# Performance work log

Measured on AMD Instinct MI355X. Metric: run time of the kernel, lower is better.

Reference implementation:

```python
import jax, jax.numpy as jnp
import numpy as np

INPUT_DIM = 1024
NUM_TARGETS = 128
BATCH = 32768


def setup_inputs() -> dict:
    key = jax.random.key(0)
    kx, kw, kb = jax.random.split(key, 3)
    x = jax.random.normal(kx, (BATCH, INPUT_DIM), dtype=jnp.float32)
    # Fused view of num_targets independent nn.Linear(input_dim, 1) layers:
    # column t of W / entry t of b are the weights/bias of layer t.
    bound = 1.0 / np.sqrt(INPUT_DIM)  # torch Linear default init range
    W = jax.random.uniform(kw, (INPUT_DIM, NUM_TARGETS), minval=-bound, maxval=bound, dtype=jnp.float32)
    b = jax.random.uniform(kb, (NUM_TARGETS,), minval=-bound, maxval=bound, dtype=jnp.float32)
    return {"x": x, "W": W, "b": b}


def reference(x, W, b):
    # Equivalent to concatenating sigmoid(Linear_t(x)) over t along last dim:
    # one fused matmul [B,D]x[D,T] + bias + sigmoid.
    return jax.nn.sigmoid(x @ W + b)
```

## Files before the change

kernel.cpp:

```cpp
#include <hip/hip_runtime.h>
#include <hip/hip_bf16.h>


typedef __bf16 bf16x8 __attribute__((ext_vector_type(8)));
typedef float  f32x4  __attribute__((ext_vector_type(4)));

#define DIM   1024
#define NT    128
#define BATCH 32768

__global__ __launch_bounds__(256) void prep_w(const float* __restrict__ W,
                                              __bf16* __restrict__ wsW) {
    int idx = blockIdx.x * 256 + threadIdx.x;
    int j = idx & 7;
    int l = (idx >> 3) & 63;
    int c = (idx >> 9) & 7;
    int s = idx >> 12;
    int k = s * 32 + (l >> 4) * 8 + j;
    int n = c * 16 + (l & 15);
    wsW[idx] = (__bf16)W[k * NT + n];
}

__global__ __launch_bounds__(256) void gemm_bias_sigmoid(
        const float* __restrict__ x,
        const __bf16* __restrict__ wsW,
        const float* __restrict__ bias,
        float* __restrict__ out) {
    const int lane = threadIdx.x & 63;
    const int wave = threadIdx.x >> 6;
    const int q    = lane >> 4;
    const int r    = lane & 15;
    const int row0 = blockIdx.x * 128 + wave * 32;

    const float* xA = x + (size_t)(row0 + r) * DIM + q * 8;
    const bf16x8* wb = (const bf16x8*)wsW + lane;

    f32x4 acc[2][8];
#pragma unroll
    for (int t = 0; t < 2; ++t)
#pragma unroll
        for (int c = 0; c < 8; ++c)
            acc[t][c] = (f32x4){0.f, 0.f, 0.f, 0.f};

    for (int s = 0; s < 32; ++s) {
        bf16x8 bfrag[8];
        const bf16x8* wp = wb + (size_t)s * 8 * 64;
#pragma unroll
        for (int c = 0; c < 8; ++c)
            bfrag[c] = wp[(size_t)c * 64];

        bf16x8 afrag[2];
#pragma unroll
        for (int t = 0; t < 2; ++t) {
            const float* ap = xA + (size_t)t * 16 * DIM + s * 32;
            float4 a0 = *(const float4*)ap;
            float4 a1 = *(const float4*)(ap + 4);
            bf16x8 af;
            af[0] = (__bf16)a0.x; af[1] = (__bf16)a0.y;
            af[2] = (__bf16)a0.z; af[3] = (__bf16)a0.w;
            af[4] = (__bf16)a1.x; af[5] = (__bf16)a1.y;
            af[6] = (__bf16)a1.z; af[7] = (__bf16)a1.w;
            afrag[t] = af;
        }

#pragma unroll
        for (int t = 0; t < 2; ++t)
#pragma unroll
            for (int c = 0; c < 8; ++c)
                acc[t][c] = __builtin_amdgcn_mfma_f32_16x16x32_bf16(
                    afrag[t], bfrag[c], acc[t][c], 0, 0, 0);
    }

#pragma unroll
    for (int t = 0; t < 2; ++t) {
#pragma unroll
        for (int c = 0; c < 8; ++c) {
            const float bv = bias[c * 16 + r];
#pragma unroll
            for (int reg = 0; reg < 4; ++reg) {
                const int row = row0 + t * 16 + q * 4 + reg;
                float v = acc[t][c][reg] + bv;
                v = 1.0f / (1.0f + __expf(-v));
                out[(size_t)row * NT + c * 16 + r] = v;
            }
        }
    }
}

extern "C" void kernel_launch(void* const* d_in, const int* in_sizes, int n_in,
                              void* d_out, int out_size, void* d_ws, size_t ws_size,
                              hipStream_t stream) {
    const float* x = (const float*)d_in[0];
    const float* W = (const float*)d_in[1];
    const float* b = (const float*)d_in[2];
    float* out     = (float*)d_out;
    __bf16* wsW    = (__bf16*)d_ws;

    prep_w<<<DIM * NT / 256, 256, 0, stream>>>(W, wsW);
    gemm_bias_sigmoid<<<BATCH / 128, 256, 0, stream>>>(x, wsW, b, out);
}
```

Before: 228.6 us.

## Shrink GEMM tiles to 16 rows per wave and double-buffer register loads

Each wave now computes 16 rows instead of 32, and blocks shrink to 2 waves covering 32 rows, so the grid grows to 1024 blocks. The main loop prefetches the next K-step's x and W fragments into a second register buffer, overlapping global loads with the MFMAs. This aims to hide memory latency and raise occupancy. The cost is that each W fragment is reused for only one row tile, doubling W traffic per output row, though W is small and likely stays in cache.

```diff
diff --git a/kernel.cpp b/kernel.cpp
--- a/kernel.cpp
+++ b/kernel.cpp
@@ -21,7 +21,7 @@
     wsW[idx] = (__bf16)W[k * NT + n];
 }
 
-__global__ __launch_bounds__(256) void gemm_bias_sigmoid(
+__global__ __launch_bounds__(128) void gemm_bias_sigmoid(
         const float* __restrict__ x,
         const __bf16* __restrict__ wsW,
         const float* __restrict__ bias,
@@ -30,59 +30,65 @@
     const int wave = threadIdx.x >> 6;
     const int q    = lane >> 4;
     const int r    = lane & 15;
-    const int row0 = blockIdx.x * 128 + wave * 32;
+    const int row0 = blockIdx.x * 32 + wave * 16;
 
     const float* xA = x + (size_t)(row0 + r) * DIM + q * 8;
     const bf16x8* wb = (const bf16x8*)wsW + lane;
 
-    f32x4 acc[2][8];
+    f32x4 acc[8];
 #pragma unroll
-    for (int t = 0; t < 2; ++t)
+    for (int c = 0; c < 8; ++c)
+        acc[c] = (f32x4){0.f, 0.f, 0.f, 0.f};
+
+    float4 abuf[2][2];
+    bf16x8 bbuf[2][8];
+
+    {
+        abuf[0][0] = *(const float4*)(xA);
+        abuf[0][1] = *(const float4*)(xA + 4);
 #pragma unroll
         for (int c = 0; c < 8; ++c)
-            acc[t][c] = (f32x4){0.f, 0.f, 0.f, 0.f};
+            bbuf[0][c] = wb[(size_t)c * 64];
+    }
 
+#pragma unroll 2
     for (int s = 0; s < 32; ++s) {
-        bf16x8 bfrag[8];
-        const bf16x8* wp = wb + (size_t)s * 8 * 64;
+        const int cur = s & 1;
+        const int nxt = cur ^ 1;
+
+        if (s < 31) {
+            const float* ap = xA + (size_t)(s + 1) * 32;
+            abuf[nxt][0] = *(const float4*)ap;
+            abuf[nxt][1] = *(const float4*)(ap + 4);
+            const bf16x8* wp = wb + (size_t)(s + 1) * 512;
+#pragma unroll
+            for (int c = 0; c < 8; ++c)
+                bbuf[nxt][c] = wp[(size_t)c * 64];
+        }
+
+        const float4 a0 = abuf[cur][0];
+        const float4 a1 = abuf[cur][1];
+        bf16x8 af;
+        af[0] = (__bf16)a0.x; af[1] = (__bf16)a0.y;
+        af[2] = (__bf16)a0.z; af[3] = (__bf16)a0.w;
+        af[4] = (__bf16)a1.x; af[5] = (__bf16)a1.y;
+        af[6] = (__bf16)a1.z; af[7] = (__bf16)a1.w;
+
 #pragma unroll
         for (int c = 0; c < 8; ++c)
-            bfrag[c] = wp[(size_t)c * 64];
-
-        bf16x8 afrag[2];
-#pragma unroll
-        for (int t = 0; t < 2; ++t) {
-            const float* ap = xA + (size_t)t * 16 * DIM + s * 32;
-            float4 a0 = *(const float4*)ap;
-            float4 a1 = *(const float4*)(ap + 4);
-            bf16x8 af;
-            af[0] = (__bf16)a0.x; af[1] = (__bf16)a0.y;
-            af[2] = (__bf16)a0.z; af[3] = (__bf16)a0.w;
-            af[4] = (__bf16)a1.x; af[5] = (__bf16)a1.y;
-            af[6] = (__bf16)a1.z; af[7] = (__bf16)a1.w;
-            afrag[t] = af;
-        }
-
-#pragma unroll
-        for (int t = 0; t < 2; ++t)
-#pragma unroll
-            for (int c = 0; c < 8; ++c)
-                acc[t][c] = __builtin_amdgcn_mfma_f32_16x16x32_bf16(
-                    afrag[t], bfrag[c], acc[t][c], 0, 0, 0);
+            acc[c] = __builtin_amdgcn_mfma_f32_16x16x32_bf16(
+                af, bbuf[cur][c], acc[c], 0, 0, 0);
     }
 
 #pragma unroll
-    for (int t = 0; t < 2; ++t) {
+    for (int c = 0; c < 8; ++c) {
+        const float bv = bias[c * 16 + r];
 #pragma unroll
-        for (int c = 0; c < 8; ++c) {
-            const float bv = bias[c * 16 + r];
-#pragma unroll
-            for (int reg = 0; reg < 4; ++reg) {
-                const int row = row0 + t * 16 + q * 4 + reg;
-                float v = acc[t][c][reg] + bv;
-                v = 1.0f / (1.0f + __expf(-v));
-                out[(size_t)row * NT + c * 16 + r] = v;
-            }
+        for (int reg = 0; reg < 4; ++reg) {
+            const int row = row0 + q * 4 + reg;
+            float v = acc[c][reg] + bv;
+            v = 1.0f / (1.0f + __expf(-v));
+            out[(size_t)row * NT + c * 16 + r] = v;
         }
     }
 }
@@ -97,5 +103,5 @@
     __bf16* wsW    = (__bf16*)d_ws;
 
     prep_w<<<DIM * NT / 256, 256, 0, stream>>>(W, wsW);
-    gemm_bias_sigmoid<<<BATCH / 128, 256, 0, stream>>>(x, wsW, b, out);
+    gemm_bias_sigmoid<<<BATCH / 32, 128, 0, stream>>>(x, wsW, b, out);
 }
```

New measurement: 423.8 us. 85.4% more time.
